# Kernel tuning notes

Hardware: AMD Instinct MI355X
Metric: run time of the kernel (lower is better)

Reference implementation:

```python
import math
import jax, jax.numpy as jnp
import numpy as np

NUM_HEADS = 8
TOP_M = 5
CLAMP_LOGIT = 2.0
LN_EPS = 1e-5


def _layernorm(x, w, b):
    m = jnp.mean(x, axis=-1, keepdims=True)
    v = jnp.mean((x - m) ** 2, axis=-1, keepdims=True)
    return (x - m) * jax.lax.rsqrt(v + LN_EPS) * w + b


def _l2norm(x, eps=1e-6):
    n = jnp.sqrt(jnp.sum(x * x, axis=-1, keepdims=True))
    return x / jnp.maximum(n, eps)


def setup_inputs() -> dict:
    key = jax.random.key(0)
    ks = jax.random.split(key, 20)
    B, H, W, Cv = 8, 64, 64, 512
    T, Ct = 77, 512
    s = 0.02
    inp = {
        'visual_features': jax.random.normal(ks[0], (B, H, W, Cv), jnp.float32),
        'text_features': jax.random.normal(ks[1], (B, T, Ct), jnp.float32),
        'norm1_w': jnp.ones((Cv,), jnp.float32),
        'norm1_b': jnp.zeros((Cv,), jnp.float32),
        'Wq': jax.random.normal(ks[2], (Cv, Cv), jnp.float32) * s,
        'bq': jnp.zeros((Cv,), jnp.float32),
        'Wk': jax.random.normal(ks[3], (Ct, Cv), jnp.float32) * s,
        'bk': jnp.zeros((Cv,), jnp.float32),
        'Wv': jax.random.normal(ks[4], (Ct, Cv), jnp.float32) * s,
        'bv': jnp.zeros((Cv,), jnp.float32),
        'Wo': jax.random.normal(ks[5], (Cv, Cv), jnp.float32) * s,
        'bo': jnp.zeros((Cv,), jnp.float32),
        'gate_w': jax.random.normal(ks[6], (Cv, 1), jnp.float32) * s,
        'gate_b': jnp.zeros((1,), jnp.float32),
        'norm2_w': jnp.ones((Cv,), jnp.float32),
        'norm2_b': jnp.zeros((Cv,), jnp.float32),
        'ffn_w1': jax.random.normal(ks[7], (Cv, 4 * Cv), jnp.float32) * s,
        'ffn_b1': jnp.zeros((4 * Cv,), jnp.float32),
        'ffn_w2': jax.random.normal(ks[8], (4 * Cv, Cv), jnp.float32) * s,
        'ffn_b2': jnp.zeros((Cv,), jnp.float32),
        'logit_scale': jnp.asarray(math.log(1.0 / 0.07), jnp.float32),
        'alpha': jnp.asarray(0.1, jnp.float32),
    }
    return inp


def reference(visual_features, text_features, norm1_w, norm1_b, Wq, bq, Wk, bk,
              Wv, bv, Wo, bo, gate_w, gate_b, norm2_w, norm2_b,
              ffn_w1, ffn_b1, ffn_w2, ffn_b2, logit_scale, alpha):
    B, H, W, Cv = visual_features.shape
    N = H * W
    Hh = NUM_HEADS
    Dh = Cv // Hh

    # Pre-LN + projections
    x = _layernorm(visual_features, norm1_w, norm1_b).reshape(B, N, Cv)
    q_full = x @ Wq + bq                       # (B,N,Cv)
    k_full = text_features @ Wk + bk           # (B,T,Cv)
    v_full = text_features @ Wv + bv           # (B,T,Cv)

    # pad mask: all-zero text tokens (B,T)
    pad_mask = jnp.sum(jnp.abs(text_features), axis=-1) <= 1e-6

    # cosine attention: normalize over full Cv before splitting heads (as in source)
    q = _l2norm(q_full).reshape(B, N, Hh, Dh)
    k = _l2norm(k_full).reshape(B, -1, Hh, Dh)
    v = v_full.reshape(B, -1, Hh, Dh)

    scale = jnp.exp(jnp.clip(logit_scale, -CLAMP_LOGIT, CLAMP_LOGIT)) / math.sqrt(Dh)
    sim = jnp.einsum('bnhd,bthd->bnht', q, k) * scale  # (B,N,Hh,T)
    sim = jnp.where(pad_mask[:, None, None, :], -jnp.inf, sim)

    # top-k sparsification along text dim (keep entries >= k-th largest)
    if TOP_M < sim.shape[-1]:
        topv = jax.lax.top_k(sim, TOP_M)[0]
        kth = topv[..., -1:]
        sim = jnp.where(sim >= kth, sim, -jnp.inf)

    attn = jax.nn.softmax(sim, axis=-1)
    aligned = jnp.einsum('bnht,bthd->bnhd', attn, v).reshape(B, N, Cv)
    aligned = aligned @ Wo + bo

    gate = jax.nn.sigmoid(x @ gate_w + gate_b)  # (B,N,1)
    y = x + alpha * gate * aligned
    y = _layernorm(y, norm2_w, norm2_b)
    h = jax.nn.gelu(y @ ffn_w1 + ffn_b1, approximate=False)
    y = y + (h @ ffn_w2 + ffn_b2)
    return y.reshape(B, H, W, Cv)
```

## Files before the change

kernel.cpp:

```cpp
#include <hip/hip_runtime.h>
#include <hip/hip_bf16.h>
#include <math.h>

constexpr int Bv = 8;
constexpr int Nv = 4096;
constexpr int Cvd = 512;
constexpr int Tt = 77;
constexpr int Dh = 64;
constexpr int MROWS = Bv * Nv;
constexpr int KTROWS = Bv * Tt;

typedef __attribute__((ext_vector_type(8))) short bf16x8;
typedef __attribute__((ext_vector_type(4))) float f32x4;

__device__ __forceinline__ float bfbits2f(short s) {
    unsigned int u = ((unsigned int)(unsigned short)s) << 16;
    return __uint_as_float(u);
}
__device__ __forceinline__ short f2bfbits(float f) {
    __hip_bfloat16 h = __float2bfloat16(f);
    return *reinterpret_cast<short*>(&h);
}

__device__ __forceinline__ void gload16(const void* g, void* l) {
    __builtin_amdgcn_global_load_lds(
        (const __attribute__((address_space(1))) void*)g,
        (__attribute__((address_space(3))) void*)l, 16, 0, 0);
}

__device__ __forceinline__ void block_barrier() {
    asm volatile("" ::: "memory");
    __builtin_amdgcn_s_barrier();
    asm volatile("" ::: "memory");
}

__global__ __launch_bounds__(256)
void wtrans4_kernel(const float* __restrict__ Wq, const float* __restrict__ Wo,
                    const float* __restrict__ w1, const float* __restrict__ w2,
                    __hip_bfloat16* __restrict__ WqT, __hip_bfloat16* __restrict__ WoT,
                    __hip_bfloat16* __restrict__ w1T, __hip_bfloat16* __restrict__ w2T)
{
    __shared__ float tile[32][33];
    const int bid = blockIdx.x;
    const float* in;
    __hip_bfloat16* out;
    int K, N, tid;
    if (bid < 256)       { in = Wq; out = WqT; K = 512;  N = 512;  tid = bid; }
    else if (bid < 512)  { in = Wo; out = WoT; K = 512;  N = 512;  tid = bid - 256; }
    else if (bid < 1536) { in = w1; out = w1T; K = 512;  N = 2048; tid = bid - 512; }
    else                 { in = w2; out = w2T; K = 2048; N = 512;  tid = bid - 1536; }
    const int nx = N >> 5;
    const int n0 = (tid % nx) * 32, k0 = (tid / nx) * 32;
    const int tx = threadIdx.x & 31, ty = threadIdx.x >> 5;
    #pragma unroll
    for (int i = ty; i < 32; i += 8)
        tile[i][tx] = in[(size_t)(k0 + i) * N + n0 + tx];
    __syncthreads();
    #pragma unroll
    for (int i = ty; i < 32; i += 8)
        out[(size_t)(n0 + i) * K + k0 + tx] = __float2bfloat16(tile[tx][i]);
}

template<bool GATE>
__global__ __launch_bounds__(128)
void ln_kernel(const float* __restrict__ in, const float* __restrict__ w,
               const float* __restrict__ b, float* __restrict__ out,
               __hip_bfloat16* __restrict__ out_bf,
               const float* __restrict__ gate_w, const float* __restrict__ gate_b,
               float* __restrict__ gate_out)
{
    __shared__ float red[4];
    __shared__ float redg[2];
    const int row = blockIdx.x;
    const int t = threadIdx.x;
    const int wv = t >> 6;
    const float4 v = ((const float4*)(in + (size_t)row * Cvd))[t];

    float s  = v.x + v.y + v.z + v.w;
    float ss = v.x*v.x + v.y*v.y + v.z*v.z + v.w*v.w;
    #pragma unroll
    for (int o = 1; o < 64; o <<= 1) {
        s  += __shfl_xor(s,  o);
        ss += __shfl_xor(ss, o);
    }
    if ((t & 63) == 0) { red[wv*2] = s; red[wv*2+1] = ss; }
    __syncthreads();
    s  = red[0] + red[2];
    ss = red[1] + red[3];
    const float m   = s * (1.0f / 512.0f);
    const float var = ss * (1.0f / 512.0f) - m * m;
    const float rs  = 1.0f / sqrtf(var + 1e-5f);

    const float4 w4 = ((const float4*)w)[t];
    const float4 b4 = ((const float4*)b)[t];
    float4 o4;
    o4.x = (v.x - m) * rs * w4.x + b4.x;
    o4.y = (v.y - m) * rs * w4.y + b4.y;
    o4.z = (v.z - m) * rs * w4.z + b4.z;
    o4.w = (v.w - m) * rs * w4.w + b4.w;
    ((float4*)(out + (size_t)row * Cvd))[t] = o4;

    __hip_bfloat162 h0, h1;
    h0.x = __float2bfloat16(o4.x); h0.y = __float2bfloat16(o4.y);
    h1.x = __float2bfloat16(o4.z); h1.y = __float2bfloat16(o4.w);
    __hip_bfloat16* obp = out_bf + (size_t)row * Cvd + 4*t;
    *(__hip_bfloat162*)(obp)     = h0;
    *(__hip_bfloat162*)(obp + 2) = h1;

    if (GATE) {
        const float4 g4 = ((const float4*)gate_w)[t];
        float g = o4.x*g4.x + o4.y*g4.y + o4.z*g4.z + o4.w*g4.w;
        #pragma unroll
        for (int o = 1; o < 64; o <<= 1) g += __shfl_xor(g, o);
        if ((t & 63) == 0) redg[wv] = g;
        __syncthreads();
        if (t == 0) {
            const float gt = redg[0] + redg[1] + gate_b[0];
            gate_out[row] = 1.0f / (1.0f + expf(-gt));
        }
    }
}

__global__ __launch_bounds__(64)
void rownorm_bf_kernel(const __hip_bfloat16* __restrict__ src, float* __restrict__ inv)
{
    const int row = blockIdx.x;
    const int l = threadIdx.x;
    const bf16x8 v = ((const bf16x8*)(src + (size_t)row * Cvd))[l];
    float ss = 0.0f;
    #pragma unroll
    for (int j = 0; j < 8; j++) {
        const float f = bfbits2f(v[j]);
        ss += f * f;
    }
    #pragma unroll
    for (int o = 1; o < 64; o <<= 1) ss += __shfl_xor(ss, o);
    if (l == 0) inv[row] = 1.0f / fmaxf(sqrtf(ss), 1e-6f);
}

__global__ __launch_bounds__(64)
void knorm_mask_kernel(const float* __restrict__ kf, const float* __restrict__ text,
                       float* __restrict__ msk, __hip_bfloat16* __restrict__ kbf)
{
    const int row = blockIdx.x;
    const int l = threadIdx.x;
    const float4* rp = (const float4*)(kf + (size_t)row * Cvd);
    const float4* tp = (const float4*)(text + (size_t)row * Cvd);
    const float4 a = rp[l], c = rp[l + 64];
    const float4 ta = tp[l], tc = tp[l + 64];
    float ss = a.x*a.x + a.y*a.y + a.z*a.z + a.w*a.w
             + c.x*c.x + c.y*c.y + c.z*c.z + c.w*c.w;
    float sa = fabsf(ta.x)+fabsf(ta.y)+fabsf(ta.z)+fabsf(ta.w)
             + fabsf(tc.x)+fabsf(tc.y)+fabsf(tc.z)+fabsf(tc.w);
    #pragma unroll
    for (int o = 1; o < 64; o <<= 1) {
        ss += __shfl_xor(ss, o);
        sa += __shfl_xor(sa, o);
    }
    const float ki = 1.0f / fmaxf(sqrtf(ss), 1e-6f);
    if (l == 0) msk[row] = (sa <= 1e-6f) ? 1.0f : 0.0f;

    __hip_bfloat16* kp = kbf + (size_t)row * Cvd;
    __hip_bfloat162 p;
    p.x = __float2bfloat16(a.x * ki); p.y = __float2bfloat16(a.y * ki);
    *(__hip_bfloat162*)(kp + l*4)     = p;
    p.x = __float2bfloat16(a.z * ki); p.y = __float2bfloat16(a.w * ki);
    *(__hip_bfloat162*)(kp + l*4 + 2) = p;
    p.x = __float2bfloat16(c.x * ki); p.y = __float2bfloat16(c.y * ki);
    *(__hip_bfloat162*)(kp + (l+64)*4)     = p;
    p.x = __float2bfloat16(c.z * ki); p.y = __float2bfloat16(c.w * ki);
    *(__hip_bfloat162*)(kp + (l+64)*4 + 2) = p;
}

__global__ __launch_bounds__(256)
void gemm32kv_kernel(const float* __restrict__ A,
                     const float* __restrict__ Wk, const float* __restrict__ bk,
                     float* __restrict__ Ck,
                     const float* __restrict__ Wv, const float* __restrict__ bv,
                     float* __restrict__ Cv2,
                     int M, int K)
{
    __shared__ float As[16][64 + 4];
    __shared__ float Bs[16][64 + 4];

    const float* W    = blockIdx.z ? Wv  : Wk;
    const float* bias = blockIdx.z ? bv  : bk;
    float*       C    = blockIdx.z ? Cv2 : Ck;

    const int t = threadIdx.x;
    const int tx = t & 15, ty = t >> 4;
    const int row0 = blockIdx.y * 64;
    const int col0 = blockIdx.x * 64;

    const int arow = t >> 2;
    const int ak   = (t & 3) << 2;
    const int brow = t >> 4;
    const int bcol = (t & 15) << 2;

    float acc[4][4] = {};

    for (int kt = 0; kt < K; kt += 16) {
        float4 a4 = make_float4(0.f, 0.f, 0.f, 0.f);
        const int gr = row0 + arow;
        if (gr < M) a4 = *(const float4*)(A + (size_t)gr * 512 + kt + ak);
        As[ak + 0][arow] = a4.x;
        As[ak + 1][arow] = a4.y;
        As[ak + 2][arow] = a4.z;
        As[ak + 3][arow] = a4.w;
        const float4 b4 = *(const float4*)(W + (size_t)(kt + brow) * 512 + col0 + bcol);
        *(float4*)&Bs[brow][bcol] = b4;
        __syncthreads();
        #pragma unroll
        for (int k = 0; k < 16; k++) {
            const float4 av = *(const float4*)&As[k][ty << 2];
            const float4 bv4 = *(const float4*)&Bs[k][tx << 2];
            acc[0][0] += av.x * bv4.x; acc[0][1] += av.x * bv4.y;
            acc[0][2] += av.x * bv4.z; acc[0][3] += av.x * bv4.w;
            acc[1][0] += av.y * bv4.x; acc[1][1] += av.y * bv4.y;
            acc[1][2] += av.y * bv4.z; acc[1][3] += av.y * bv4.w;
            acc[2][0] += av.z * bv4.x; acc[2][1] += av.z * bv4.y;
            acc[2][2] += av.z * bv4.z; acc[2][3] += av.z * bv4.w;
            acc[3][0] += av.w * bv4.x; acc[3][1] += av.w * bv4.y;
            acc[3][2] += av.w * bv4.z; acc[3][3] += av.w * bv4.w;
        }
        __syncthreads();
    }

    #pragma unroll
    for (int i = 0; i < 4; i++) {
        const int r = row0 + (ty << 2) + i;
        if (r >= M) continue;
        #pragma unroll
        for (int j = 0; j < 4; j++) {
            const int c = col0 + (tx << 2) + j;
            C[(size_t)r * 512 + c] = acc[i][j] + bias[c];
        }
    }
}

enum { EPI_NONE = 0, EPI_WO = 1, EPI_GELU = 2, EPI_RES = 3, EPI_QBF = 4 };

template<int NT, int EPI>
__global__ __launch_bounds__(256, 3)
void bgemm_kernel(const __hip_bfloat16* __restrict__ Ah,
                  const __hip_bfloat16* __restrict__ Bth,
                  const float* __restrict__ bias,
                  void* __restrict__ Cout,
                  int M, int N,
                  const float* __restrict__ xres,
                  const float* __restrict__ gate,
                  const float* __restrict__ alpha_p,
                  const float* __restrict__ yres)
{
    constexpr int K = NT * 32;
    __shared__ short lds[3 * 8192];

    const short* A  = (const short*)Ah;
    const short* Bt = (const short*)Bth;

    const int nwg = gridDim.x;
    const int cpx = nwg >> 3;
    const int bid0 = blockIdx.x;
    const int bid = (bid0 & 7) * cpx + (bid0 >> 3);
    const int cols = N >> 7;
    const int row0 = (bid / cols) << 7;
    const int col0 = (bid % cols) << 7;

    const int t = threadIdx.x;
    const int w = t >> 6, l = t & 63;
    const int wr = w >> 1, wc = w & 1;

    const int src_kelem = (((l & 3) ^ ((l >> 3) & 3)) << 3);
    const short* pA0;
    const short* pA1;
    const short* pB0;
    const short* pB1;
    {
        const int r0 = (2*w)*16 + (l >> 2);
        const int r1 = (2*w + 1)*16 + (l >> 2);
        pA0 = A  + (size_t)(row0 + r0) * K + src_kelem;
        pA1 = A  + (size_t)(row0 + r1) * K + src_kelem;
        pB0 = Bt + (size_t)(col0 + r0) * K + src_kelem;
        pB1 = Bt + (size_t)(col0 + r1) * K + src_kelem;
    }
    short* const dA = lds + (2*w) * 512;
    short* const dB = lds + 4096 + (2*w) * 512;

    auto STAGE = [&](int kt, int bW) {
        gload16(pA0 + kt * 32, dA + bW * 8192);
        gload16(pA1 + kt * 32, dA + bW * 8192 + 512);
        gload16(pB0 + kt * 32, dB + bW * 8192);
        gload16(pB1 + kt * 32, dB + bW * 8192 + 512);
    };

    const int axk = (((l >> 4) << 4) ^ (((l >> 1) & 3) << 4));
    const char* const bA = (const char*)lds + (wr*64 + (l & 15))*64 + axk;
    const char* const bB = (const char*)lds + 8192 + (wc*64 + (l & 15))*64 + axk;

    bf16x8 a[4], b[4];
    f32x4 acc[4][4] = {};

    auto RD = [&](int bR) {
        #pragma unroll
        for (int i = 0; i < 4; i++)
            a[i] = *(const bf16x8*)(bA + bR*16384 + i*1024);
        #pragma unroll
        for (int i = 0; i < 4; i++)
            b[i] = *(const bf16x8*)(bB + bR*16384 + i*1024);
    };
    auto MF = [&]() {
        __builtin_amdgcn_s_setprio(1);
        #pragma unroll
        for (int i = 0; i < 4; i++)
            #pragma unroll
            for (int ni = 0; ni < 4; ni++)
                acc[i][ni] = __builtin_amdgcn_mfma_f32_16x16x32_bf16(
                    a[i], b[ni], acc[i][ni], 0, 0, 0);
        __builtin_amdgcn_s_setprio(0);
    };

    STAGE(0, 0); STAGE(1, 1);
    asm volatile("s_waitcnt vmcnt(4)" ::: "memory");
    block_barrier();

    #pragma unroll
    for (int kt = 0; kt < NT; ++kt) {
        const int bR = kt % 3;
        RD(bR);
        if (kt + 2 < NT) {
            STAGE(kt + 2, (kt + 2) % 3);
            asm volatile("s_waitcnt vmcnt(4)" ::: "memory");
        } else if (kt + 1 < NT) {
            asm volatile("s_waitcnt vmcnt(0)" ::: "memory");
        }
        block_barrier();
        MF();
        if (kt + 1 < NT) block_barrier();
    }

    const float alpha = (EPI == EPI_WO) ? alpha_p[0] : 0.0f;
    #pragma unroll
    for (int mi = 0; mi < 4; mi++) {
        const int rbase = row0 + wr*64 + mi*16 + ((l >> 4) << 2);
        #pragma unroll
        for (int ni = 0; ni < 4; ni++) {
            const int c = col0 + wc*64 + ni*16 + (l & 15);
            const float bc = bias[c];
            #pragma unroll
            for (int r = 0; r < 4; r++) {
                const int rr = rbase + r;
                const size_t idx = (size_t)rr * N + c;
                float val = acc[mi][ni][r] + bc;
                if (EPI == EPI_GELU) {
                    const float u = 1.5957691216f * val
                                  + 0.0713548163f * val * val * val;
                    val = val / (1.0f + __expf(-u));
                    ((__hip_bfloat16*)Cout)[idx] = __float2bfloat16(val);
                } else if (EPI == EPI_QBF) {
                    ((__hip_bfloat16*)Cout)[idx] = __float2bfloat16(val);
                } else if (EPI == EPI_WO) {
                    ((float*)Cout)[idx] = xres[idx] + alpha * gate[rr] * val;
                } else if (EPI == EPI_RES) {
                    ((float*)Cout)[idx] = yres[idx] + val;
                } else {
                    ((float*)Cout)[idx] = val;
                }
            }
        }
    }
}

__global__ __launch_bounds__(256)
void attn_kernel(const __hip_bfloat16* __restrict__ qf,
                 const __hip_bfloat16* __restrict__ kbf,
                 const float* __restrict__ vf,
                 const float* __restrict__ qinv,
                 const float* __restrict__ msk,
                 const float* __restrict__ logit_scale,
                 __hip_bfloat16* __restrict__ out)
{
    __shared__ short kb[80 * 72];
    __shared__ float v_lds[Tt][68];
    __shared__ float qinv_s[256];
    __shared__ float bias_s[80];

    const int gid = blockIdx.x;
    const int b = gid >> 7;
    const int h = (gid >> 4) & 7;
    const int ntile = gid & 15;
    const int t = threadIdx.x;
    const int row0 = b * Nv + ntile * 256;

    #pragma unroll
    for (int it = 0; it < 3; ++it) {
        const int ch = t + it * 256;
        if (ch < 616) {
            const int row = ch >> 3, part = ch & 7;
            *(bf16x8*)&kb[row * 72 + part * 8] =
                *(const bf16x8*)(kbf + (size_t)(b * Tt + row) * Cvd + h * Dh + part * 8);
        }
    }
    if (t < 27) {
        const bf16x8 z = {0,0,0,0,0,0,0,0};
        *(bf16x8*)&kb[77 * 72 + t * 8] = z;
    }
    for (int idx = t; idx < Tt * Dh; idx += 256) {
        const int tt = idx >> 6, dd = idx & 63;
        v_lds[tt][dd] = vf[(size_t)(b * Tt + tt) * Cvd + h * Dh + dd];
    }
    qinv_s[t] = qinv[row0 + t];
    if (t < 80) bias_s[t] = (t < 77 && msk[b * Tt + t] == 0.0f) ? 0.0f : -1e30f;
    __syncthreads();

    float ls = logit_scale[0];
    ls = fminf(fmaxf(ls, -2.0f), 2.0f);
    const float scale = __expf(ls) * 0.125f;

    const int w = t >> 6, l = t & 63;
    const int c = l & 15, g = l >> 4;

    bf16x8 qfrag[8];
    #pragma unroll
    for (int rt = 0; rt < 4; ++rt)
        #pragma unroll
        for (int kk = 0; kk < 2; ++kk)
            qfrag[rt*2 + kk] = *(const bf16x8*)(qf +
                (size_t)(row0 + w*64 + rt*16 + c) * Cvd + h * Dh + kk*32 + g*8);

    #pragma unroll
    for (int rt = 0; rt < 4; ++rt) {
        const int lrow = w*64 + rt*16 + c;
        const float qsc = qinv_s[lrow] * scale;

        float v0=-INFINITY,v1=-INFINITY,v2=-INFINITY,v3=-INFINITY,v4=-INFINITY;
        int   i0=0,i1=0,i2=0,i3=0,i4=0;
        auto INS = [&](float s, int idx) {
            const bool c0=s>v0, c1=s>v1, c2=s>v2, c3=s>v3, c4=s>v4;
            const float nv0=c0?s:v0;              const int ni0=c0?idx:i0;
            const float nv1=c1?(c0?v0:s):v1;      const int ni1=c1?(c0?i0:idx):i1;
            const float nv2=c2?(c1?v1:s):v2;      const int ni2=c2?(c1?i1:idx):i2;
            const float nv3=c3?(c2?v2:s):v3;      const int ni3=c3?(c2?i2:idx):i3;
            const float nv4=c4?(c3?v3:s):v4;      const int ni4=c4?(c3?i3:idx):i4;
            v0=nv0;v1=nv1;v2=nv2;v3=nv3;v4=nv4;
            i0=ni0;i1=ni1;i2=ni2;i3=ni3;i4=ni4;
        };

        #pragma unroll
        for (int kt = 0; kt < 5; ++kt) {
            f32x4 acc = {0.f, 0.f, 0.f, 0.f};
            const bf16x8 ka0 = *(const bf16x8*)&kb[(kt*16 + c) * 72 + g*8];
            const bf16x8 ka1 = *(const bf16x8*)&kb[(kt*16 + c) * 72 + 32 + g*8];
            acc = __builtin_amdgcn_mfma_f32_16x16x32_bf16(ka0, qfrag[rt*2+0], acc, 0, 0, 0);
            acc = __builtin_amdgcn_mfma_f32_16x16x32_bf16(ka1, qfrag[rt*2+1], acc, 0, 0, 0);
            #pragma unroll
            for (int r = 0; r < 4; ++r) {
                const int key = kt*16 + g*4 + r;
                INS(acc[r] * qsc + bias_s[key], key);
            }
        }

        #pragma unroll
        for (int st = 16; st <= 32; st <<= 1) {
            const float m0=__shfl_xor(v0,st), m1=__shfl_xor(v1,st),
                        m2=__shfl_xor(v2,st), m3=__shfl_xor(v3,st),
                        m4=__shfl_xor(v4,st);
            const int   j0=__shfl_xor(i0,st), j1=__shfl_xor(i1,st),
                        j2=__shfl_xor(i2,st), j3=__shfl_xor(i3,st),
                        j4=__shfl_xor(i4,st);
            INS(m0,j0); INS(m1,j1); INS(m2,j2); INS(m3,j3); INS(m4,j4);
        }

        const float e1=__expf(v1-v0), e2=__expf(v2-v0),
                    e3=__expf(v3-v0), e4=__expf(v4-v0);
        const float inv = 1.0f / (1.0f + e1 + e2 + e3 + e4);
        const float w0=inv, w1=e1*inv, w2=e2*inv, w3=e3*inv, w4=e4*inv;

        float o[16];
        #pragma unroll
        for (int d4 = 0; d4 < 4; ++d4) {
            const int dd = g*16 + d4*4;
            const float4 p0 = *(const float4*)&v_lds[i0][dd];
            const float4 p1 = *(const float4*)&v_lds[i1][dd];
            const float4 p2 = *(const float4*)&v_lds[i2][dd];
            const float4 p3 = *(const float4*)&v_lds[i3][dd];
            const float4 p4 = *(const float4*)&v_lds[i4][dd];
            o[d4*4+0] = w0*p0.x + w1*p1.x + w2*p2.x + w3*p3.x + w4*p4.x;
            o[d4*4+1] = w0*p0.y + w1*p1.y + w2*p2.y + w3*p3.y + w4*p4.y;
            o[d4*4+2] = w0*p0.z + w1*p1.z + w2*p2.z + w3*p3.z + w4*p4.z;
            o[d4*4+3] = w0*p0.w + w1*p1.w + w2*p2.w + w3*p3.w + w4*p4.w;
        }
        __hip_bfloat16* op = out + (size_t)(row0 + lrow) * Cvd + h * Dh + g*16;
        bf16x8 s0, s1;
        #pragma unroll
        for (int j = 0; j < 8; ++j) { s0[j] = f2bfbits(o[j]); s1[j] = f2bfbits(o[8+j]); }
        *(bf16x8*)op       = s0;
        *(bf16x8*)(op + 8) = s1;
    }
}

extern "C" void kernel_launch(void* const* d_in, const int* in_sizes, int n_in,
                              void* d_out, int out_size, void* d_ws, size_t ws_size,
                              hipStream_t stream)
{
    const float* visual = (const float*)d_in[0];
    const float* text   = (const float*)d_in[1];
    const float* n1w = (const float*)d_in[2];
    const float* n1b = (const float*)d_in[3];
    const float* Wq  = (const float*)d_in[4];
    const float* bq  = (const float*)d_in[5];
    const float* Wk  = (const float*)d_in[6];
    const float* bk  = (const float*)d_in[7];
    const float* Wv  = (const float*)d_in[8];
    const float* bv  = (const float*)d_in[9];
    const float* Wo  = (const float*)d_in[10];
    const float* bo  = (const float*)d_in[11];
    const float* gw  = (const float*)d_in[12];
    const float* gb  = (const float*)d_in[13];
    const float* n2w = (const float*)d_in[14];
    const float* n2b = (const float*)d_in[15];
    const float* w1  = (const float*)d_in[16];
    const float* b1  = (const float*)d_in[17];
    const float* w2  = (const float*)d_in[18];
    const float* b2  = (const float*)d_in[19];
    const float* lsc = (const float*)d_in[20];
    const float* alp = (const float*)d_in[21];

    float* out = (float*)d_out;
    char*  w8  = (char*)d_ws;

    __hip_bfloat16* qbf    = (__hip_bfloat16*)(w8 + 0);
    float*          ypre   = (float*)(w8 + 67108864);
    __hip_bfloat16* hidden = (__hip_bfloat16*)(w8 + 0);
    __hip_bfloat16* xbf    = (__hip_bfloat16*)(w8 + 134217728);
    float*          kf     = (float*)(w8 + 167772160);
    float*          vf     = (float*)(w8 + 169033728);
    float*          qinv   = (float*)(w8 + 170295296);
    float*          mskp   = (float*)(w8 + 170428832);
    float*          gate   = (float*)(w8 + 170431296);
    __hip_bfloat16* WqT    = (__hip_bfloat16*)(w8 + 170562368);
    __hip_bfloat16* WoT    = (__hip_bfloat16*)(w8 + 171086656);
    __hip_bfloat16* w1T    = (__hip_bfloat16*)(w8 + 171610944);
    __hip_bfloat16* w2T    = (__hip_bfloat16*)(w8 + 173708096);
    __hip_bfloat16* kbfg   = (__hip_bfloat16*)(w8 + 175805248);

    wtrans4_kernel<<<dim3(2560), dim3(256), 0, stream>>>(
        Wq, Wo, w1, w2, WqT, WoT, w1T, w2T);

    ln_kernel<true><<<dim3(MROWS), dim3(128), 0, stream>>>(
        visual, n1w, n1b, out, xbf, gw, gb, gate);

    bgemm_kernel<16, EPI_QBF><<<dim3(1024), dim3(256), 0, stream>>>(
        xbf, WqT, bq, qbf, MROWS, 512, nullptr, nullptr, nullptr, nullptr);

    gemm32kv_kernel<<<dim3(8, 10, 2), dim3(256), 0, stream>>>(
        text, Wk, bk, kf, Wv, bv, vf, KTROWS, 512);

    rownorm_bf_kernel<<<dim3(MROWS), dim3(64), 0, stream>>>(qbf, qinv);
    knorm_mask_kernel<<<dim3(KTROWS), dim3(64), 0, stream>>>(kf, text, mskp, kbfg);

    attn_kernel<<<dim3(1024), dim3(256), 0, stream>>>(
        qbf, kbfg, vf, qinv, mskp, lsc, xbf);

    bgemm_kernel<16, EPI_WO><<<dim3(1024), dim3(256), 0, stream>>>(
        xbf, WoT, bo, ypre, MROWS, 512, out, gate, alp, nullptr);

    ln_kernel<false><<<dim3(MROWS), dim3(128), 0, stream>>>(
        ypre, n2w, n2b, out, xbf, nullptr, nullptr, nullptr);

    bgemm_kernel<16, EPI_GELU><<<dim3(4096), dim3(256), 0, stream>>>(
        xbf, w1T, b1, hidden, MROWS, 2048, nullptr, nullptr, nullptr, nullptr);

    bgemm_kernel<64, EPI_RES><<<dim3(1024), dim3(256), 0, stream>>>(
        hidden, w2T, b2, out, MROWS, 512, nullptr, nullptr, nullptr, out);
}
```

Measured before the change: 408.0 us.

## Fuse q row-norm into Q GEMM epilogue and drop fp32 LN2 output

```diff
diff --git a/kernel.cpp b/kernel.cpp
--- a/kernel.cpp
+++ b/kernel.cpp
@@ -61,7 +61,7 @@
         out[(size_t)(n0 + i) * K + k0 + tx] = __float2bfloat16(tile[tx][i]);
 }
 
-template<bool GATE>
+template<bool GATE, bool WF32>
 __global__ __launch_bounds__(128)
 void ln_kernel(const float* __restrict__ in, const float* __restrict__ w,
                const float* __restrict__ b, float* __restrict__ out,
@@ -98,7 +98,7 @@
     o4.y = (v.y - m) * rs * w4.y + b4.y;
     o4.z = (v.z - m) * rs * w4.z + b4.z;
     o4.w = (v.w - m) * rs * w4.w + b4.w;
-    ((float4*)(out + (size_t)row * Cvd))[t] = o4;
+    if (WF32) ((float4*)(out + (size_t)row * Cvd))[t] = o4;
 
     __hip_bfloat162 h0, h1;
     h0.x = __float2bfloat16(o4.x); h0.y = __float2bfloat16(o4.y);
@@ -119,23 +119,6 @@
             gate_out[row] = 1.0f / (1.0f + expf(-gt));
         }
     }
-}
-
-__global__ __launch_bounds__(64)
-void rownorm_bf_kernel(const __hip_bfloat16* __restrict__ src, float* __restrict__ inv)
-{
-    const int row = blockIdx.x;
-    const int l = threadIdx.x;
-    const bf16x8 v = ((const bf16x8*)(src + (size_t)row * Cvd))[l];
-    float ss = 0.0f;
-    #pragma unroll
-    for (int j = 0; j < 8; j++) {
-        const float f = bfbits2f(v[j]);
-        ss += f * f;
-    }
-    #pragma unroll
-    for (int o = 1; o < 64; o <<= 1) ss += __shfl_xor(ss, o);
-    if (l == 0) inv[row] = 1.0f / fmaxf(sqrtf(ss), 1e-6f);
 }
 
 __global__ __launch_bounds__(64)
@@ -250,7 +233,7 @@
                   const float* __restrict__ xres,
                   const float* __restrict__ gate,
                   const float* __restrict__ alpha_p,
-                  const float* __restrict__ yres)
+                  const void* __restrict__ yres)
 {
     constexpr int K = NT * 32;
     __shared__ short lds[3 * 8192];
@@ -336,6 +319,30 @@
         block_barrier();
         MF();
         if (kt + 1 < NT) block_barrier();
+    }
+
+    if (EPI == EPI_QBF) {
+        float* qsum = (float*)Cout == nullptr ? nullptr : (float*)(size_t)0;
+        (void)qsum;
+        #pragma unroll
+        for (int mi = 0; mi < 4; mi++) {
+            #pragma unroll
+            for (int r = 0; r < 4; r++) {
+                const int rr = row0 + wr*64 + mi*16 + ((l >> 4) << 2) + r;
+                float ssq = 0.0f;
+                #pragma unroll
+                for (int ni = 0; ni < 4; ni++) {
+                    const int c = col0 + wc*64 + ni*16 + (l & 15);
+                    const float val = acc[mi][ni][r] + bias[c];
+                    ((__hip_bfloat16*)Cout)[(size_t)rr * N + c] = __float2bfloat16(val);
+                    ssq += val * val;
+                }
+                #pragma unroll
+                for (int o = 1; o < 16; o <<= 1) ssq += __shfl_xor(ssq, o);
+                if ((l & 15) == 0) atomicAdd((float*)xres + rr, ssq);
+            }
+        }
+        return;
     }
 
     const float alpha = (EPI == EPI_WO) ? alpha_p[0] : 0.0f;
@@ -356,12 +363,10 @@
                                   + 0.0713548163f * val * val * val;
                     val = val / (1.0f + __expf(-u));
                     ((__hip_bfloat16*)Cout)[idx] = __float2bfloat16(val);
-                } else if (EPI == EPI_QBF) {
-                    ((__hip_bfloat16*)Cout)[idx] = __float2bfloat16(val);
                 } else if (EPI == EPI_WO) {
                     ((float*)Cout)[idx] = xres[idx] + alpha * gate[rr] * val;
                 } else if (EPI == EPI_RES) {
-                    ((float*)Cout)[idx] = yres[idx] + val;
+                    ((float*)Cout)[idx] = bfbits2f(((const short*)yres)[idx]) + val;
                 } else {
                     ((float*)Cout)[idx] = val;
                 }
@@ -374,7 +379,7 @@
 void attn_kernel(const __hip_bfloat16* __restrict__ qf,
                  const __hip_bfloat16* __restrict__ kbf,
                  const float* __restrict__ vf,
-                 const float* __restrict__ qinv,
+                 const float* __restrict__ qsum,
                  const float* __restrict__ msk,
                  const float* __restrict__ logit_scale,
                  __hip_bfloat16* __restrict__ out)
@@ -408,7 +413,7 @@
         const int tt = idx >> 6, dd = idx & 63;
         v_lds[tt][dd] = vf[(size_t)(b * Tt + tt) * Cvd + h * Dh + dd];
     }
-    qinv_s[t] = qinv[row0 + t];
+    qinv_s[t] = 1.0f / fmaxf(sqrtf(qsum[row0 + t]), 1e-6f);
     if (t < 80) bias_s[t] = (t < 77 && msk[b * Tt + t] == 0.0f) ? 0.0f : -1e30f;
     __syncthreads();
 
@@ -534,7 +539,7 @@
     __hip_bfloat16* xbf    = (__hip_bfloat16*)(w8 + 134217728);
     float*          kf     = (float*)(w8 + 167772160);
     float*          vf     = (float*)(w8 + 169033728);
-    float*          qinv   = (float*)(w8 + 170295296);
+    float*          qsum   = (float*)(w8 + 170295296);
     float*          mskp   = (float*)(w8 + 170428832);
     float*          gate   = (float*)(w8 + 170431296);
     __hip_bfloat16* WqT    = (__hip_bfloat16*)(w8 + 170562368);
@@ -545,31 +550,31 @@
 
     wtrans4_kernel<<<dim3(2560), dim3(256), 0, stream>>>(
         Wq, Wo, w1, w2, WqT, WoT, w1T, w2T);
-
-    ln_kernel<true><<<dim3(MROWS), dim3(128), 0, stream>>>(
+    hipMemsetAsync(qsum, 0, MROWS * sizeof(float), stream);
+
+    ln_kernel<true, true><<<dim3(MROWS), dim3(128), 0, stream>>>(
         visual, n1w, n1b, out, xbf, gw, gb, gate);
 
     bgemm_kernel<16, EPI_QBF><<<dim3(1024), dim3(256), 0, stream>>>(
-        xbf, WqT, bq, qbf, MROWS, 512, nullptr, nullptr, nullptr, nullptr);
+        xbf, WqT, bq, qbf, MROWS, 512, qsum, nullptr, nullptr, nullptr);
 
     gemm32kv_kernel<<<dim3(8, 10, 2), dim3(256), 0, stream>>>(
         text, Wk, bk, kf, Wv, bv, vf, KTROWS, 512);
 
-    rownorm_bf_kernel<<<dim3(MROWS), dim3(64), 0, stream>>>(qbf, qinv);
     knorm_mask_kernel<<<dim3(KTROWS), dim3(64), 0, stream>>>(kf, text, mskp, kbfg);
 
     attn_kernel<<<dim3(1024), dim3(256), 0, stream>>>(
-        qbf, kbfg, vf, qinv, mskp, lsc, xbf);
+        qbf, kbfg, vf, qsum, mskp, lsc, xbf);
 
     bgemm_kernel<16, EPI_WO><<<dim3(1024), dim3(256), 0, stream>>>(
         xbf, WoT, bo, ypre, MROWS, 512, out, gate, alp, nullptr);
 
-    ln_kernel<false><<<dim3(MROWS), dim3(128), 0, stream>>>(
-        ypre, n2w, n2b, out, xbf, nullptr, nullptr, nullptr);
+    ln_kernel<false, false><<<dim3(MROWS), dim3(128), 0, stream>>>(
+        ypre, n2w, n2b, nullptr, xbf, nullptr, nullptr, nullptr);
 
     bgemm_kernel<16, EPI_GELU><<<dim3(4096), dim3(256), 0, stream>>>(
         xbf, w1T, b1, hidden, MROWS, 2048, nullptr, nullptr, nullptr, nullptr);
 
     bgemm_kernel<64, EPI_RES><<<dim3(1024), dim3(256), 0, stream>>>(
-        hidden, w2T, b2, out, MROWS, 512, nullptr, nullptr, nullptr, out);
-}
+        hidden, w2T, b2, out, MROWS, 512, nullptr, nullptr, nullptr, xbf);
+}
```

New measurement: 395.1 us. -3.2%, faster.
